# Optimization experiments

Measured on AMD Instinct MI355X. Metric: run time of the kernel, lower is better.

## Reference

```python
import jax, jax.numpy as jnp
import numpy as np

DIM = 512
D = 256
SCALE = D ** (-0.5)


def setup_inputs() -> dict:
    key = jax.random.key(0)
    ks = jax.random.split(key, 7)
    B, N, K = 16, 4096, 32
    g = 0.1 * (6.0 / (DIM + D)) ** 0.5  # xavier_uniform with gain=0.1
    return {
        "E_patches": jax.random.normal(ks[0], (B, N, DIM), jnp.float32),
        "T_b5": jax.random.normal(ks[1], (B, K, DIM), jnp.float32),
        "P_batch": jax.random.uniform(ks[2], (B, N), jnp.float32),
        "Wq": jax.random.uniform(ks[3], (D, DIM), jnp.float32, -g, g),
        "Wk": jax.random.uniform(ks[4], (D, DIM), jnp.float32, -g, g),
        "Wv": jax.random.uniform(ks[5], (D, DIM), jnp.float32, -g, g),
        "Wo": jax.random.uniform(ks[6], (DIM, D), jnp.float32, -g, g),
    }


def reference(E_patches, T_b5, P_batch, Wq, Wk, Wv, Wo):
    # Projections (torch Linear: x @ W.T)
    Q = jnp.einsum('bkm,dm->bkd', T_b5, Wq)       # [B,K,D]
    Kp = jnp.einsum('bnm,dm->bnd', E_patches, Wk)  # [B,N,D]
    V = jnp.einsum('bnm,dm->bnd', E_patches, Wv)   # [B,N,D]
    scores = jnp.einsum('bkd,bnd->bkn', Q, Kp) * SCALE
    logP = jnp.log(jnp.clip(P_batch, 0.1, 0.9))    # [B,N]
    scores = scores + logP[:, None, :]             # additive log-prior bias
    A = jax.nn.softmax(scores, axis=-1)            # [B,K,N]
    F_agg = jnp.einsum('bkn,bnd->bkd', A, V)
    F_agg = jnp.einsum('bkd,md->bkm', F_agg, Wo)   # [B,K,DIM]
    F_agg = F_agg / (jnp.linalg.norm(F_agg, axis=-1, keepdims=True) + 1e-8)
    return (F_agg, A)
```

## Files before the change

### kernel.cpp

```cpp
#include <hip/hip_runtime.h>

typedef __bf16 bf16x8 __attribute__((ext_vector_type(8)));
typedef __bf16 bf16x4 __attribute__((ext_vector_type(4)));
typedef float  f32x4  __attribute__((ext_vector_type(4)));

__device__ __forceinline__ void cp16(void* lds, const void* g) {
  __builtin_amdgcn_global_load_lds(
      (const __attribute__((address_space(1))) unsigned int*)g,
      (__attribute__((address_space(3))) unsigned int*)lds, 16, 0, 0);
}

#define VMCNT16 asm volatile("s_waitcnt vmcnt(16)" ::: "memory")
#define VMCNT0  asm volatile("s_waitcnt vmcnt(0)" ::: "memory")
#define LGKM0   asm volatile("s_waitcnt lgkmcnt(0)" ::: "memory")
#define BARRAW  __builtin_amdgcn_s_barrier
#define MFMA    __builtin_amdgcn_mfma_f32_16x16x32_bf16


__global__ __launch_bounds__(256) void cvt_small(const float* __restrict__ Wq,
                                                 const float* __restrict__ Wk,
                                                 const float* __restrict__ Wv,
                                                 const float* __restrict__ Wo,
                                                 const float* __restrict__ T,
                                                 __bf16* __restrict__ Wqb,
                                                 __bf16* __restrict__ Tbf,
                                                 __bf16* __restrict__ WkT,
                                                 float* __restrict__ WvT,
                                                 float* __restrict__ WoT) {
  const int idx = blockIdx.x * 256 + threadIdx.x;
  if (idx < 32768) {
    const int o = idx * 4;
    f32x4 v = *(const f32x4*)(Wq + o);
    bf16x4 b;
    b[0] = (__bf16)v[0]; b[1] = (__bf16)v[1];
    b[2] = (__bf16)v[2]; b[3] = (__bf16)v[3];
    *(bf16x4*)(Wqb + o) = b;
  } else if (idx < 98304) {
    const int o = (idx - 32768) * 4;
    f32x4 v = *(const f32x4*)(T + o);
    bf16x4 b;
    b[0] = (__bf16)v[0]; b[1] = (__bf16)v[1];
    b[2] = (__bf16)v[2]; b[3] = (__bf16)v[3];
    *(bf16x4*)(Tbf + o) = b;
  } else if (idx < 106496) {
    const int t2 = idx - 98304;
    const int d0 = (t2 >> 7) * 4, m0 = (t2 & 127) * 4;
    f32x4 r0 = *(const f32x4*)(Wk + (size_t)(d0 + 0) * 512 + m0);
    f32x4 r1 = *(const f32x4*)(Wk + (size_t)(d0 + 1) * 512 + m0);
    f32x4 r2 = *(const f32x4*)(Wk + (size_t)(d0 + 2) * 512 + m0);
    f32x4 r3 = *(const f32x4*)(Wk + (size_t)(d0 + 3) * 512 + m0);
#pragma unroll
    for (int j = 0; j < 4; ++j) {
      bf16x4 o;
      o[0] = (__bf16)r0[j]; o[1] = (__bf16)r1[j];
      o[2] = (__bf16)r2[j]; o[3] = (__bf16)r3[j];
      *(bf16x4*)(WkT + (size_t)(m0 + j) * 256 + d0) = o;
    }
  } else if (idx < 114688) {
    const int t2 = idx - 106496;
    const int d0 = (t2 >> 7) * 4, m0 = (t2 & 127) * 4;
    f32x4 r0 = *(const f32x4*)(Wv + (size_t)(d0 + 0) * 512 + m0);
    f32x4 r1 = *(const f32x4*)(Wv + (size_t)(d0 + 1) * 512 + m0);
    f32x4 r2 = *(const f32x4*)(Wv + (size_t)(d0 + 2) * 512 + m0);
    f32x4 r3 = *(const f32x4*)(Wv + (size_t)(d0 + 3) * 512 + m0);
#pragma unroll
    for (int j = 0; j < 4; ++j) {
      f32x4 o;
      o[0] = r0[j]; o[1] = r1[j]; o[2] = r2[j]; o[3] = r3[j];
      *(f32x4*)(WvT + (size_t)(m0 + j) * 256 + d0) = o;
    }
  } else {
    const int t2 = idx - 114688;
    const int m0 = (t2 >> 6) * 4, d0 = (t2 & 63) * 4;
    f32x4 r0 = *(const f32x4*)(Wo + (size_t)(m0 + 0) * 256 + d0);
    f32x4 r1 = *(const f32x4*)(Wo + (size_t)(m0 + 1) * 256 + d0);
    f32x4 r2 = *(const f32x4*)(Wo + (size_t)(m0 + 2) * 256 + d0);
    f32x4 r3 = *(const f32x4*)(Wo + (size_t)(m0 + 3) * 256 + d0);
#pragma unroll
    for (int j = 0; j < 4; ++j) {
      f32x4 o;
      o[0] = r0[j]; o[1] = r1[j]; o[2] = r2[j]; o[3] = r3[j];
      *(f32x4*)(WoT + (size_t)(d0 + j) * 512 + m0) = o;
    }
  }
}

__global__ __launch_bounds__(256) void qproj(const __bf16* __restrict__ Wqb,
                                             const __bf16* __restrict__ Tbf,
                                             __bf16* __restrict__ Qw) {
  __shared__ __align__(16) __bf16 At[4096];
  __shared__ __align__(16) __bf16 Bt[4096];
  const int tid = threadIdx.x, lane = tid & 63;
  const int q = lane >> 4, ln = lane & 15;
  const int w = tid >> 6, wm = w >> 1, wn = w & 1;
  const int t = blockIdx.x;
  const int nbase = (t & 3) * 128;
  const int mbase = (t >> 2) * 128;
  f32x4 acc[4][4] = {};
  for (int kt = 0; kt < 16; ++kt) {
    const int k0 = kt * 32;
    __syncthreads();
#pragma unroll
    for (int s = 0; s < 2; ++s) {
      const int cbase = (tid & 192) + s * 256;
      const int cc = cbase + lane;
      const int row = cc >> 2, kc = (cc & 3) * 8;
      cp16(&At[cbase * 8], Wqb + (size_t)(mbase + row) * 512 + k0 + kc);
      cp16(&Bt[cbase * 8], Tbf + (size_t)(nbase + row) * 512 + k0 + kc);
    }
    __syncthreads();
    bf16x8 af[4], bfr[4];
#pragma unroll
    for (int f = 0; f < 4; ++f) {
      af[f]  = *(const bf16x8*)&At[(wm * 64 + f * 16 + ln) * 32 + q * 8];
      bfr[f] = *(const bf16x8*)&Bt[(wn * 64 + f * 16 + ln) * 32 + q * 8];
    }
#pragma unroll
    for (int fm = 0; fm < 4; ++fm)
#pragma unroll
      for (int fn = 0; fn < 4; ++fn)
        acc[fm][fn] = MFMA(af[fm], bfr[fn], acc[fm][fn], 0, 0, 0);
  }
#pragma unroll
  for (int fm = 0; fm < 4; ++fm)
#pragma unroll
    for (int fn = 0; fn < 4; ++fn) {
      const int m = mbase + wm * 64 + fm * 16 + q * 4;
      const int n = nbase + wn * 64 + fn * 16 + ln;
      f32x4 v = acc[fm][fn];
      bf16x4 o;
      o[0] = (__bf16)v[0]; o[1] = (__bf16)v[1];
      o[2] = (__bf16)v[2]; o[3] = (__bf16)v[3];
      *(bf16x4*)&Qw[(size_t)n * 256 + m] = o;
    }
}

__global__ __launch_bounds__(256) void qwk(const __bf16* __restrict__ WkT,
                                           const __bf16* __restrict__ Qwp,
                                           __bf16* __restrict__ QWkb) {
  __shared__ __align__(16) __bf16 At[4096];
  __shared__ __align__(16) __bf16 Bt[4096];
  const int tid = threadIdx.x, lane = tid & 63;
  const int q = lane >> 4, ln = lane & 15;
  const int w = tid >> 6, wm = w >> 1, wn = w & 1;
  const int t = blockIdx.x;
  const int nbase = (t & 3) * 128;
  const int mbase = (t >> 2) * 128;
  f32x4 acc[4][4] = {};
  for (int kt = 0; kt < 8; ++kt) {
    const int k0 = kt * 32;
    __syncthreads();
#pragma unroll
    for (int s = 0; s < 2; ++s) {
      const int cbase = (tid & 192) + s * 256;
      const int cc = cbase + lane;
      const int row = cc >> 2, kc = (cc & 3) * 8;
      cp16(&At[cbase * 8], WkT + (size_t)(mbase + row) * 256 + k0 + kc);
      cp16(&Bt[cbase * 8], Qwp + (size_t)(nbase + row) * 256 + k0 + kc);
    }
    __syncthreads();
    bf16x8 af[4], bfr[4];
#pragma unroll
    for (int f = 0; f < 4; ++f) {
      af[f]  = *(const bf16x8*)&At[(wm * 64 + f * 16 + ln) * 32 + q * 8];
      bfr[f] = *(const bf16x8*)&Bt[(wn * 64 + f * 16 + ln) * 32 + q * 8];
    }
#pragma unroll
    for (int fm = 0; fm < 4; ++fm)
#pragma unroll
      for (int fn = 0; fn < 4; ++fn)
        acc[fm][fn] = MFMA(af[fm], bfr[fn], acc[fm][fn], 0, 0, 0);
  }
#pragma unroll
  for (int fm = 0; fm < 4; ++fm)
#pragma unroll
    for (int fn = 0; fn < 4; ++fn) {
      const int m = mbase + wm * 64 + fm * 16 + q * 4;
      const int n = nbase + wn * 64 + fn * 16 + ln;
      f32x4 v = acc[fm][fn];
      bf16x4 o;
      o[0] = (__bf16)v[0]; o[1] = (__bf16)v[1];
      o[2] = (__bf16)v[2]; o[3] = (__bf16)v[3];
      *(bf16x4*)&QWkb[(size_t)n * 512 + m] = o;
    }
}

__device__ __forceinline__ void load_e(f32x4 (&ev)[16], const float* Eb,
                                       int s, int rg, int cg0) {
#pragma unroll
  for (int i = 0; i < 4; ++i) {
    const int cg = cg0 + i * 32;
#pragma unroll
    for (int r = 0; r < 4; ++r)
      ev[i * 4 + r] = *(const f32x4*)(Eb + (size_t)(s * 64 + rg * 4 + r) * 512 + cg * 4);
  }
}
__device__ __forceinline__ void cvtwrite_e(const f32x4 (&ev)[16], __bf16* Er,
                                           __bf16* EtT, int rg, int cg0) {
#pragma unroll
  for (int i = 0; i < 4; ++i) {
    const int cg = cg0 + i * 32;
#pragma unroll
    for (int r = 0; r < 4; ++r) {
      bf16x4 rw;
      rw[0] = (__bf16)ev[i*4+r][0]; rw[1] = (__bf16)ev[i*4+r][1];
      rw[2] = (__bf16)ev[i*4+r][2]; rw[3] = (__bf16)ev[i*4+r][3];
      *(bf16x4*)((char*)Er + (size_t)(rg * 4 + r) * 1040 + cg * 8) = rw;
    }
#pragma unroll
    for (int j = 0; j < 4; ++j) {
      bf16x4 tw;
      tw[0] = (__bf16)ev[i*4+0][j]; tw[1] = (__bf16)ev[i*4+1][j];
      tw[2] = (__bf16)ev[i*4+2][j]; tw[3] = (__bf16)ev[i*4+3][j];
      const int m = cg * 4 + j;
      const int u = (rg >> 1) ^ ((m >> 3) & 7);
      *(bf16x4*)((char*)EtT + (size_t)m * 144 + u * 16 + (rg & 1) * 8) = tw;
    }
  }
}
__device__ __forceinline__ void phase1(int s, const bf16x8 (&qf)[16],
                                       const __bf16* Er, __bf16* Plds,
                                       const float* Lp, float* rsum,
                                       int kf, int nf, int q, int ln) {
  f32x4 sacc = {0.f, 0.f, 0.f, 0.f};
#pragma unroll
  for (int kk = 0; kk < 16; ++kk) {
    bf16x8 bb = *(const bf16x8*)((char*)Er + (size_t)(nf * 16 + ln) * 1040 + kk * 64 + q * 16);
    sacc = MFMA(qf[kk], bb, sacc, 0, 0, 0);
  }
  const float lp = Lp[s * 64 + nf * 16 + ln];
  float pv[4];
#pragma unroll
  for (int r = 0; r < 4; ++r) {
    pv[r] = __expf(sacc[r] * 0.0625f + lp);
    Plds[(kf * 16 + q * 4 + r) * 72 + nf * 16 + ln] = (__bf16)pv[r];
  }
#pragma unroll
  for (int mm = 1; mm < 16; mm <<= 1)
#pragma unroll
    for (int r = 0; r < 4; ++r) pv[r] += __shfl_xor(pv[r], mm, 64);
  if (ln == 0) {
#pragma unroll
    for (int r = 0; r < 4; ++r) atomicAdd(&rsum[kf * 16 + q * 4 + r], pv[r]);
  }
}
__device__ __forceinline__ void phase2a(f32x4 (&facc)[2][4], const __bf16* Plds,
                                        const __bf16* EtT, int w, int q, int ln,
                                        int tid, bf16x4* pr) {
#pragma unroll
  for (int kkn = 0; kkn < 2; ++kkn) {
    bf16x8 pa0 = *(const bf16x8*)((char*)Plds + (size_t)(ln) * 144 + kkn * 64 + q * 16);
    bf16x8 pa1 = *(const bf16x8*)((char*)Plds + (size_t)(16 + ln) * 144 + kkn * 64 + q * 16);
#pragma unroll
    for (int mf = 0; mf < 4; ++mf) {
      const int m = w * 64 + mf * 16 + ln;
      const int u = (kkn * 4 + q) ^ ((m >> 3) & 7);
      bf16x8 vb = *(const bf16x8*)((char*)EtT + (size_t)m * 144 + u * 16);
      facc[0][mf] = MFMA(pa0, vb, facc[0][mf], 0, 0, 0);
      facc[1][mf] = MFMA(pa1, vb, facc[1][mf], 0, 0, 0);
    }
  }
  *pr = *(const bf16x4*)((char*)Plds + (size_t)(tid >> 4) * 144 + (tid & 15) * 8);
}

__global__ __launch_bounds__(512, 2) void fused_main(
    const float* __restrict__ E, const __bf16* __restrict__ QWkb,
    const float* __restrict__ Pb, __bf16* __restrict__ Pws,
    float* __restrict__ Fpart, float* __restrict__ rowsum) {
  __shared__ __align__(16) __bf16 Er[64 * 520];
  __shared__ __align__(16) __bf16 EtT[512 * 72];
  __shared__ __align__(16) __bf16 Plds[32 * 72];
  __shared__ __align__(16) float Lp[256];
  __shared__ float rsum[32];

  const int tid = threadIdx.x;
  const int lane = tid & 63;
  const int q = lane >> 4, ln = lane & 15;
  const int w = tid >> 6;
  const int kf = w >> 2;
  const int nf = w & 3;
  const int b = blockIdx.y, c = blockIdx.x;
  const int rg = tid >> 5;
  const int cg0 = tid & 31;

  const float* Eb = E + ((size_t)b * 4096 + (size_t)c * 256) * 512;

  bf16x8 qf[16];
  {
    const __bf16* qr = QWkb + (size_t)(b * 32 + kf * 16 + ln) * 512 + q * 8;
#pragma unroll
    for (int kk = 0; kk < 16; ++kk) qf[kk] = *(const bf16x8*)(qr + kk * 32);
  }
  if (tid < 256) {
    float p = Pb[b * 4096 + c * 256 + tid];
    Lp[tid] = __logf(fminf(fmaxf(p, 0.1f), 0.9f));
  }
  if (tid < 32) rsum[tid] = 0.f;

  f32x4 evA[16], evB[16];
  load_e(evA, Eb, 0, rg, cg0);
  load_e(evB, Eb, 1, rg, cg0);
  VMCNT16;
  cvtwrite_e(evA, Er, EtT, rg, cg0);
  load_e(evA, Eb, 2, rg, cg0);
  LGKM0; BARRAW();

  f32x4 facc[2][4] = {};
  bf16x4 pr0, pr1, pr2, pr3;

  phase1(0, qf, Er, Plds, Lp, rsum, kf, nf, q, ln);
  LGKM0; BARRAW();
  phase2a(facc, Plds, EtT, w, q, ln, tid, &pr0);
  BARRAW();
  VMCNT16;
  cvtwrite_e(evB, Er, EtT, rg, cg0);
  load_e(evB, Eb, 3, rg, cg0);
  LGKM0; BARRAW();
  phase1(1, qf, Er, Plds, Lp, rsum, kf, nf, q, ln);
  LGKM0; BARRAW();
  phase2a(facc, Plds, EtT, w, q, ln, tid, &pr1);
  BARRAW();
  VMCNT16;
  cvtwrite_e(evA, Er, EtT, rg, cg0);
  LGKM0; BARRAW();
  phase1(2, qf, Er, Plds, Lp, rsum, kf, nf, q, ln);
  LGKM0; BARRAW();
  phase2a(facc, Plds, EtT, w, q, ln, tid, &pr2);
  BARRAW();
  VMCNT0;
  cvtwrite_e(evB, Er, EtT, rg, cg0);
  LGKM0; BARRAW();
  phase1(3, qf, Er, Plds, Lp, rsum, kf, nf, q, ln);
  LGKM0; BARRAW();
  phase2a(facc, Plds, EtT, w, q, ln, tid, &pr3);

  {
    const int k = tid >> 4, j = (tid & 15) * 4;
    __bf16* pwr = Pws + (size_t)(b * 32 + k) * 4096 + c * 256 + j;
    *(bf16x4*)(pwr)       = pr0;
    *(bf16x4*)(pwr + 64)  = pr1;
    *(bf16x4*)(pwr + 128) = pr2;
    *(bf16x4*)(pwr + 192) = pr3;
  }
  float* Fp = Fpart + ((size_t)c * 512 + b * 32) * 512;
#pragma unroll
  for (int kf2 = 0; kf2 < 2; ++kf2)
#pragma unroll
    for (int mf = 0; mf < 4; ++mf)
#pragma unroll
      for (int r = 0; r < 4; ++r)
        Fp[(size_t)(kf2 * 16 + q * 4 + r) * 512 + w * 64 + mf * 16 + ln] = facc[kf2][mf][r];
  if (tid < 32) atomicAdd(&rowsum[b * 32 + tid], rsum[tid]);
}

__global__ __launch_bounds__(256) void norm_p(const __bf16* __restrict__ Pws,
                                              const float* __restrict__ rowsum,
                                              float* __restrict__ Aout) {
  const size_t idx = ((size_t)blockIdx.x * 256 + threadIdx.x) * 4;
  const int row = (int)(idx >> 12);
  const float invs = 1.0f / rowsum[row];
  bf16x4 p = *(const bf16x4*)(Pws + idx);
  f32x4 o;
  o[0] = (float)p[0] * invs; o[1] = (float)p[1] * invs;
  o[2] = (float)p[2] * invs; o[3] = (float)p[3] * invs;
  *(f32x4*)(Aout + idx) = o;
}

__global__ __launch_bounds__(256) void final_kernel(const float* __restrict__ Fpart,
                                                    const float* __restrict__ WvT,
                                                    const float* __restrict__ WoT,
                                                    float* __restrict__ Fout) {
  __shared__ float fl[512];
  __shared__ float agg[256];
  __shared__ float f2b[512];
  __shared__ float redbuf[4];
  const int row = blockIdx.x;
  const int t = threadIdx.x;
  const int lane = t & 63;
  const int w = t >> 6;

  {
    float s0 = 0.f, s1 = 0.f;
#pragma unroll
    for (int cc = 0; cc < 16; ++cc) {
      const float* p = Fpart + (size_t)cc * 262144 + (size_t)row * 512;
      s0 += p[t]; s1 += p[t + 256];
    }
    fl[t] = s0; fl[t + 256] = s1;
  }
  __syncthreads();

  {
    float a0 = 0.f, a1 = 0.f, a2 = 0.f, a3 = 0.f;
    for (int m = 0; m < 512; m += 4) {
      a0 += fl[m]     * WvT[(size_t)(m + 0) * 256 + t];
      a1 += fl[m + 1] * WvT[(size_t)(m + 1) * 256 + t];
      a2 += fl[m + 2] * WvT[(size_t)(m + 2) * 256 + t];
      a3 += fl[m + 3] * WvT[(size_t)(m + 3) * 256 + t];
    }
    agg[t] = (a0 + a1) + (a2 + a3);
  }
  __syncthreads();

  {
    float b0 = 0.f, b1 = 0.f, b2 = 0.f, b3 = 0.f;
    float c0 = 0.f, c1 = 0.f, c2 = 0.f, c3 = 0.f;
    for (int d = 0; d < 256; d += 4) {
      const float g0 = agg[d], g1 = agg[d + 1], g2 = agg[d + 2], g3 = agg[d + 3];
      b0 += g0 * WoT[(size_t)(d + 0) * 512 + t];
      b1 += g1 * WoT[(size_t)(d + 1) * 512 + t];
      b2 += g2 * WoT[(size_t)(d + 2) * 512 + t];
      b3 += g3 * WoT[(size_t)(d + 3) * 512 + t];
      c0 += g0 * WoT[(size_t)(d + 0) * 512 + t + 256];
      c1 += g1 * WoT[(size_t)(d + 1) * 512 + t + 256];
      c2 += g2 * WoT[(size_t)(d + 2) * 512 + t + 256];
      c3 += g3 * WoT[(size_t)(d + 3) * 512 + t + 256];
    }
    f2b[t] = (b0 + b1) + (b2 + b3);
    f2b[t + 256] = (c0 + c1) + (c2 + c3);
  }
  __syncthreads();

  {
    const float x0 = f2b[t], x1 = f2b[t + 256];
    float ps = x0 * x0 + x1 * x1;
#pragma unroll
    for (int mm = 1; mm < 64; mm <<= 1) ps += __shfl_xor(ps, mm, 64);
    if (lane == 0) redbuf[w] = ps;
  }
  __syncthreads();
  {
    const float tot = redbuf[0] + redbuf[1] + redbuf[2] + redbuf[3];
    const float sc = 1.0f / (sqrtf(tot) + 1e-8f);
    Fout[(size_t)row * 512 + t] = f2b[t] * sc;
    Fout[(size_t)row * 512 + t + 256] = f2b[t + 256] * sc;
  }
}

extern "C" void kernel_launch(void* const* d_in, const int* in_sizes, int n_in,
                              void* d_out, int out_size, void* d_ws, size_t ws_size,
                              hipStream_t stream) {
  const float* E  = (const float*)d_in[0];
  const float* T  = (const float*)d_in[1];
  const float* Pb = (const float*)d_in[2];
  const float* Wq = (const float*)d_in[3];
  const float* Wk = (const float*)d_in[4];
  const float* Wv = (const float*)d_in[5];
  const float* Wo = (const float*)d_in[6];

  float* out  = (float*)d_out;
  float* Fout = out;
  float* Aout = out + 262144;

  char* ws = (char*)d_ws;
  float*  Fpart = (float*)ws;
  __bf16* Pws   = (__bf16*)(ws + 16777216);
  __bf16* Tbf   = (__bf16*)(ws + 20971520);
  __bf16* Wqb   = (__bf16*)(ws + 21495808);
  __bf16* WkT   = (__bf16*)(ws + 21757952);
  float*  WvT   = (float*)(ws + 22020096);
  __bf16* Qw    = (__bf16*)(ws + 22544384);
  __bf16* QWkb  = (__bf16*)(ws + 22806528);
  float*  rowsum = (float*)(ws + 23330816);
  float*  WoT   = (float*)(ws + 23332864);

  hipMemsetAsync(rowsum, 0, 2048, stream);

  cvt_small<<<480, 256, 0, stream>>>(Wq, Wk, Wv, Wo, T, Wqb, Tbf, WkT, WvT, WoT);
  qproj<<<8, 256, 0, stream>>>(Wqb, Tbf, Qw);
  qwk<<<16, 256, 0, stream>>>(WkT, Qw, QWkb);
  fused_main<<<dim3(16, 16), 512, 0, stream>>>(E, QWkb, Pb, Pws, Fpart, rowsum);
  norm_p<<<2048, 256, 0, stream>>>(Pws, rowsum, Aout);
  final_kernel<<<512, 256, 0, stream>>>(Fpart, WvT, WoT, Fout);
}
```

Before: 276.3 us.

## Split fused attention into 512 smaller 256-thread blocks over 128-row chunks

The main fused kernel now runs 32x16 blocks of 256 threads, each covering 128 patch rows in 32-row steps, instead of 16x16 blocks of 512 threads covering 256 rows. The intent is to fill more of the GPU's compute units, since 256 blocks is about the CU count, and to shrink per-block LDS so more blocks fit per CU. In exchange, register double-buffering of E loads is dropped in favour of a single buffer with full vmcnt waits, each wave does twice as many output MFMA columns, and the Fpart partial sums double so final_kernel reduces over 32 chunks instead of 16.

```diff
diff --git a/kernel.cpp b/kernel.cpp
--- a/kernel.cpp
+++ b/kernel.cpp
@@ -10,7 +10,6 @@
       (__attribute__((address_space(3))) unsigned int*)lds, 16, 0, 0);
 }
 
-#define VMCNT16 asm volatile("s_waitcnt vmcnt(16)" ::: "memory")
 #define VMCNT0  asm volatile("s_waitcnt vmcnt(0)" ::: "memory")
 #define LGKM0   asm volatile("s_waitcnt lgkmcnt(0)" ::: "memory")
 #define BARRAW  __builtin_amdgcn_s_barrier
@@ -192,11 +191,11 @@
     const int cg = cg0 + i * 32;
 #pragma unroll
     for (int r = 0; r < 4; ++r)
-      ev[i * 4 + r] = *(const f32x4*)(Eb + (size_t)(s * 64 + rg * 4 + r) * 512 + cg * 4);
+      ev[i * 4 + r] = *(const f32x4*)(Eb + (size_t)(s * 32 + rg * 4 + r) * 512 + cg * 4);
   }
 }
 __device__ __forceinline__ void cvtwrite_e(const f32x4 (&ev)[16], __bf16* Er,
-                                           __bf16* EtT, int rg, int cg0) {
+                                           char* EtT, int rg, int cg0) {
 #pragma unroll
   for (int i = 0; i < 4; ++i) {
     const int cg = cg0 + i * 32;
@@ -213,8 +212,8 @@
       tw[0] = (__bf16)ev[i*4+0][j]; tw[1] = (__bf16)ev[i*4+1][j];
       tw[2] = (__bf16)ev[i*4+2][j]; tw[3] = (__bf16)ev[i*4+3][j];
       const int m = cg * 4 + j;
-      const int u = (rg >> 1) ^ ((m >> 3) & 7);
-      *(bf16x4*)((char*)EtT + (size_t)m * 144 + u * 16 + (rg & 1) * 8) = tw;
+      const int u = (rg >> 1) ^ (m & 3);
+      *(bf16x4*)(EtT + (size_t)m * 80 + u * 16 + (rg & 1) * 8) = tw;
     }
   }
 }
@@ -228,12 +227,12 @@
     bf16x8 bb = *(const bf16x8*)((char*)Er + (size_t)(nf * 16 + ln) * 1040 + kk * 64 + q * 16);
     sacc = MFMA(qf[kk], bb, sacc, 0, 0, 0);
   }
-  const float lp = Lp[s * 64 + nf * 16 + ln];
+  const float lp = Lp[s * 32 + nf * 16 + ln];
   float pv[4];
 #pragma unroll
   for (int r = 0; r < 4; ++r) {
     pv[r] = __expf(sacc[r] * 0.0625f + lp);
-    Plds[(kf * 16 + q * 4 + r) * 72 + nf * 16 + ln] = (__bf16)pv[r];
+    *((__bf16*)((char*)Plds + (size_t)(kf * 16 + q * 4 + r) * 80) + nf * 16 + ln) = (__bf16)pv[r];
   }
 #pragma unroll
   for (int mm = 1; mm < 16; mm <<= 1)
@@ -244,46 +243,43 @@
     for (int r = 0; r < 4; ++r) atomicAdd(&rsum[kf * 16 + q * 4 + r], pv[r]);
   }
 }
-__device__ __forceinline__ void phase2a(f32x4 (&facc)[2][4], const __bf16* Plds,
-                                        const __bf16* EtT, int w, int q, int ln,
-                                        int tid, bf16x4* pr) {
-#pragma unroll
-  for (int kkn = 0; kkn < 2; ++kkn) {
-    bf16x8 pa0 = *(const bf16x8*)((char*)Plds + (size_t)(ln) * 144 + kkn * 64 + q * 16);
-    bf16x8 pa1 = *(const bf16x8*)((char*)Plds + (size_t)(16 + ln) * 144 + kkn * 64 + q * 16);
-#pragma unroll
-    for (int mf = 0; mf < 4; ++mf) {
-      const int m = w * 64 + mf * 16 + ln;
-      const int u = (kkn * 4 + q) ^ ((m >> 3) & 7);
-      bf16x8 vb = *(const bf16x8*)((char*)EtT + (size_t)m * 144 + u * 16);
-      facc[0][mf] = MFMA(pa0, vb, facc[0][mf], 0, 0, 0);
-      facc[1][mf] = MFMA(pa1, vb, facc[1][mf], 0, 0, 0);
-    }
-  }
-  *pr = *(const bf16x4*)((char*)Plds + (size_t)(tid >> 4) * 144 + (tid & 15) * 8);
-}
-
-__global__ __launch_bounds__(512, 2) void fused_main(
+__device__ __forceinline__ void phase2(f32x4 (&facc)[2][8], const __bf16* Plds,
+                                       const char* EtT, int w, int q, int ln,
+                                       int tid, bf16x4* pr) {
+  bf16x8 pa0 = *(const bf16x8*)((char*)Plds + (size_t)(ln) * 80 + q * 16);
+  bf16x8 pa1 = *(const bf16x8*)((char*)Plds + (size_t)(16 + ln) * 80 + q * 16);
+#pragma unroll
+  for (int mf = 0; mf < 8; ++mf) {
+    const int m = w * 128 + mf * 16 + ln;
+    const int u = q ^ (m & 3);
+    bf16x8 vb = *(const bf16x8*)(EtT + (size_t)m * 80 + u * 16);
+    facc[0][mf] = MFMA(pa0, vb, facc[0][mf], 0, 0, 0);
+    facc[1][mf] = MFMA(pa1, vb, facc[1][mf], 0, 0, 0);
+  }
+  *pr = *(const bf16x4*)((char*)Plds + (size_t)(tid >> 3) * 80 + (tid & 7) * 8);
+}
+
+__global__ __launch_bounds__(256, 2) void fused_main(
     const float* __restrict__ E, const __bf16* __restrict__ QWkb,
     const float* __restrict__ Pb, __bf16* __restrict__ Pws,
     float* __restrict__ Fpart, float* __restrict__ rowsum) {
-  __shared__ __align__(16) __bf16 Er[64 * 520];
-  __shared__ __align__(16) __bf16 EtT[512 * 72];
-  __shared__ __align__(16) __bf16 Plds[32 * 72];
-  __shared__ __align__(16) float Lp[256];
+  __shared__ __align__(16) __bf16 Er[32 * 520];
+  __shared__ __align__(16) char  EtT[512 * 80];
+  __shared__ __align__(16) __bf16 Plds[32 * 40];
+  __shared__ __align__(16) float Lp[128];
   __shared__ float rsum[32];
 
   const int tid = threadIdx.x;
   const int lane = tid & 63;
   const int q = lane >> 4, ln = lane & 15;
   const int w = tid >> 6;
-  const int kf = w >> 2;
-  const int nf = w & 3;
+  const int kf = w >> 1;
+  const int nf = w & 1;
   const int b = blockIdx.y, c = blockIdx.x;
   const int rg = tid >> 5;
   const int cg0 = tid & 31;
 
-  const float* Eb = E + ((size_t)b * 4096 + (size_t)c * 256) * 512;
+  const float* Eb = E + ((size_t)b * 4096 + (size_t)c * 128) * 512;
 
   bf16x8 qf[16];
   {
@@ -291,65 +287,65 @@
 #pragma unroll
     for (int kk = 0; kk < 16; ++kk) qf[kk] = *(const bf16x8*)(qr + kk * 32);
   }
-  if (tid < 256) {
-    float p = Pb[b * 4096 + c * 256 + tid];
+  if (tid < 128) {
+    float p = Pb[b * 4096 + c * 128 + tid];
     Lp[tid] = __logf(fminf(fmaxf(p, 0.1f), 0.9f));
   }
   if (tid < 32) rsum[tid] = 0.f;
 
-  f32x4 evA[16], evB[16];
-  load_e(evA, Eb, 0, rg, cg0);
-  load_e(evB, Eb, 1, rg, cg0);
-  VMCNT16;
-  cvtwrite_e(evA, Er, EtT, rg, cg0);
-  load_e(evA, Eb, 2, rg, cg0);
-  LGKM0; BARRAW();
-
-  f32x4 facc[2][4] = {};
+  f32x4 ev[16];
+  load_e(ev, Eb, 0, rg, cg0);
+
+  f32x4 facc[2][8] = {};
   bf16x4 pr0, pr1, pr2, pr3;
 
+  VMCNT0;
+  cvtwrite_e(ev, Er, EtT, rg, cg0);
+  load_e(ev, Eb, 1, rg, cg0);
+  LGKM0; BARRAW();
   phase1(0, qf, Er, Plds, Lp, rsum, kf, nf, q, ln);
   LGKM0; BARRAW();
-  phase2a(facc, Plds, EtT, w, q, ln, tid, &pr0);
-  BARRAW();
-  VMCNT16;
-  cvtwrite_e(evB, Er, EtT, rg, cg0);
-  load_e(evB, Eb, 3, rg, cg0);
-  LGKM0; BARRAW();
-  phase1(1, qf, Er, Plds, Lp, rsum, kf, nf, q, ln);
-  LGKM0; BARRAW();
-  phase2a(facc, Plds, EtT, w, q, ln, tid, &pr1);
-  BARRAW();
-  VMCNT16;
-  cvtwrite_e(evA, Er, EtT, rg, cg0);
-  LGKM0; BARRAW();
-  phase1(2, qf, Er, Plds, Lp, rsum, kf, nf, q, ln);
-  LGKM0; BARRAW();
-  phase2a(facc, Plds, EtT, w, q, ln, tid, &pr2);
+  phase2(facc, Plds, EtT, w, q, ln, tid, &pr0);
   BARRAW();
   VMCNT0;
-  cvtwrite_e(evB, Er, EtT, rg, cg0);
+  cvtwrite_e(ev, Er, EtT, rg, cg0);
+  load_e(ev, Eb, 2, rg, cg0);
+  LGKM0; BARRAW();
+  phase1(1, qf, Er, Plds, Lp, rsum, kf, nf, q, ln);
+  LGKM0; BARRAW();
+  phase2(facc, Plds, EtT, w, q, ln, tid, &pr1);
+  BARRAW();
+  VMCNT0;
+  cvtwrite_e(ev, Er, EtT, rg, cg0);
+  load_e(ev, Eb, 3, rg, cg0);
+  LGKM0; BARRAW();
+  phase1(2, qf, Er, Plds, Lp, rsum, kf, nf, q, ln);
+  LGKM0; BARRAW();
+  phase2(facc, Plds, EtT, w, q, ln, tid, &pr2);
+  BARRAW();
+  VMCNT0;
+  cvtwrite_e(ev, Er, EtT, rg, cg0);
   LGKM0; BARRAW();
   phase1(3, qf, Er, Plds, Lp, rsum, kf, nf, q, ln);
   LGKM0; BARRAW();
-  phase2a(facc, Plds, EtT, w, q, ln, tid, &pr3);
-
-  {
-    const int k = tid >> 4, j = (tid & 15) * 4;
-    __bf16* pwr = Pws + (size_t)(b * 32 + k) * 4096 + c * 256 + j;
-    *(bf16x4*)(pwr)       = pr0;
-    *(bf16x4*)(pwr + 64)  = pr1;
-    *(bf16x4*)(pwr + 128) = pr2;
-    *(bf16x4*)(pwr + 192) = pr3;
+  phase2(facc, Plds, EtT, w, q, ln, tid, &pr3);
+
+  {
+    const int prow = tid >> 3, pc = (tid & 7) * 4;
+    __bf16* pwr = Pws + (size_t)(b * 32 + prow) * 4096 + c * 128 + pc;
+    *(bf16x4*)(pwr)      = pr0;
+    *(bf16x4*)(pwr + 32) = pr1;
+    *(bf16x4*)(pwr + 64) = pr2;
+    *(bf16x4*)(pwr + 96) = pr3;
   }
   float* Fp = Fpart + ((size_t)c * 512 + b * 32) * 512;
 #pragma unroll
   for (int kf2 = 0; kf2 < 2; ++kf2)
 #pragma unroll
-    for (int mf = 0; mf < 4; ++mf)
+    for (int mf = 0; mf < 8; ++mf)
 #pragma unroll
       for (int r = 0; r < 4; ++r)
-        Fp[(size_t)(kf2 * 16 + q * 4 + r) * 512 + w * 64 + mf * 16 + ln] = facc[kf2][mf][r];
+        Fp[(size_t)(kf2 * 16 + q * 4 + r) * 512 + w * 128 + mf * 16 + ln] = facc[kf2][mf][r];
   if (tid < 32) atomicAdd(&rowsum[b * 32 + tid], rsum[tid]);
 }
 
@@ -382,7 +378,7 @@
   {
     float s0 = 0.f, s1 = 0.f;
 #pragma unroll
-    for (int cc = 0; cc < 16; ++cc) {
+    for (int cc = 0; cc < 32; ++cc) {
       const float* p = Fpart + (size_t)cc * 262144 + (size_t)row * 512;
       s0 += p[t]; s1 += p[t + 256];
     }
@@ -454,22 +450,22 @@
 
   char* ws = (char*)d_ws;
   float*  Fpart = (float*)ws;
-  __bf16* Pws   = (__bf16*)(ws + 16777216);
-  __bf16* Tbf   = (__bf16*)(ws + 20971520);
-  __bf16* Wqb   = (__bf16*)(ws + 21495808);
-  __bf16* WkT   = (__bf16*)(ws + 21757952);
-  float*  WvT   = (float*)(ws + 22020096);
-  __bf16* Qw    = (__bf16*)(ws + 22544384);
-  __bf16* QWkb  = (__bf16*)(ws + 22806528);
-  float*  rowsum = (float*)(ws + 23330816);
-  float*  WoT   = (float*)(ws + 23332864);
+  __bf16* Pws   = (__bf16*)(ws + 33554432);
+  __bf16* Tbf   = (__bf16*)(ws + 37748736);
+  __bf16* Wqb   = (__bf16*)(ws + 38273024);
+  __bf16* WkT   = (__bf16*)(ws + 38535168);
+  float*  WvT   = (float*)(ws + 38797312);
+  __bf16* Qw    = (__bf16*)(ws + 39321600);
+  __bf16* QWkb  = (__bf16*)(ws + 39583744);
+  float*  rowsum = (float*)(ws + 40108032);
+  float*  WoT   = (float*)(ws + 40110080);
 
   hipMemsetAsync(rowsum, 0, 2048, stream);
 
   cvt_small<<<480, 256, 0, stream>>>(Wq, Wk, Wv, Wo, T, Wqb, Tbf, WkT, WvT, WoT);
   qproj<<<8, 256, 0, stream>>>(Wqb, Tbf, Qw);
   qwk<<<16, 256, 0, stream>>>(WkT, Qw, QWkb);
-  fused_main<<<dim3(16, 16), 512, 0, stream>>>(E, QWkb, Pb, Pws, Fpart, rowsum);
+  fused_main<<<dim3(32, 16), 256, 0, stream>>>(E, QWkb, Pb, Pws, Fpart, rowsum);
   norm_p<<<2048, 256, 0, stream>>>(Pws, rowsum, Aout);
   final_kernel<<<512, 256, 0, stream>>>(Fpart, WvT, WoT, Fout);
 }
```

New measurement: 268.2 us (median of 2 runs). 2.9% less time.
